# Kernel tuning notes

Measured on AMD Instinct MI355X. Metric: run time of the kernel, lower is better.

## Reference

```python
import jax, jax.numpy as jnp
import numpy as np

SHIFT = 8  # shift_range init kwarg
EPS = 1e-12  # F.normalize default eps (x / max(||x||, eps))


def setup_inputs() -> dict:
    key = jax.random.key(0)
    k1, k2 = jax.random.split(key)
    grd_feature = jax.random.normal(k1, (64, 64, 24, 24), dtype=jnp.float32)
    sat_feature = jax.random.normal(k2, (64, 64, 64, 64), dtype=jnp.float32)
    return {"grd_feature": grd_feature, "sat_feature": sat_feature}


def reference(grd_feature, sat_feature):
    M, C, Hs, Ws = sat_feature.shape
    N, _, H, W = grd_feature.shape
    kH = min(H, Hs - 2 * SHIFT, 24)
    kW = min(W, Ws - 2 * SHIFT, 24)
    # center-crop ground features to kernel size
    grd = grd_feature[:, :, H // 2 - kH // 2: H // 2 + kH // 2,
                      W // 2 - kW // 2: W // 2 + kW // 2]  # [N,C,kH,kW]
    # crop sat features to search window (kernel + 2*shift)
    sat = sat_feature[:, :, Hs // 2 - SHIFT - kH // 2: Hs // 2 + SHIFT + kH // 2,
                      Ws // 2 - SHIFT - kW // 2: Ws // 2 + SHIFT + kW // 2]  # [M,C,Hi,Wi]
    # cross-correlation: repeat+grouped-conv in torch == plain conv2d here -> [M,N,Ho,Wo]
    corr = jax.lax.conv_general_dilated(
        sat, grd, window_strides=(1, 1), padding='VALID',
        dimension_numbers=('NCHW', 'OIHW', 'NCHW'))
    Ho, Wo = corr.shape[2], corr.shape[3]
    flat_idx = jnp.argmax(corr.reshape(M, N, Ho * Wo), axis=-1)  # [M,N]
    hy = flat_idx // Wo
    wx = flat_idx % Wo

    def gather_patch(sat_j, h, w):  # sat_j: [C,Hi,Wi]
        return jax.lax.dynamic_slice(sat_j, (0, h, w), (C, kH, kW))

    # vectorized patch gather over (M, N) -> [M,N,C,kH,kW]
    patches = jax.vmap(
        lambda sj, hs, ws: jax.vmap(lambda h, w: gather_patch(sj, h, w))(hs, ws)
    )(sat, hy, wx)

    pn = patches.reshape(M * N, -1)
    pn = pn / jnp.maximum(jnp.linalg.norm(pn, axis=-1, keepdims=True), EPS)
    pn = pn.reshape(M, N, C, kH, kW)
    gn = grd.reshape(N, -1)
    gn = gn / jnp.maximum(jnp.linalg.norm(gn, axis=-1, keepdims=True), EPS)
    gn = gn.reshape(N, C, kH, kW)
    similarity_matrix = jnp.einsum('mnchw,nchw->mn', pn, gn)
    sat_f = patches[M - 1, N - 1]  # last gathered (unnormalized) patch, as in torch
    return similarity_matrix, sat_f
```

## Files before the change

kernel.cpp:

```cpp
#include <hip/hip_runtime.h>
#include <hip/hip_bf16.h>
#include <math.h>


typedef float f32x16 __attribute__((ext_vector_type(16)));
typedef short short8 __attribute__((ext_vector_type(8)));

#define SATT_H 0u
#define GRDT_H 3276800u
#define CORR_O 4456448u
#define WING_O 5701632u
#define GN2_O  5702016u
#define CEX_O  5702144u
#define S2G_O  5702528u

__global__ __launch_bounds__(256) void prep(const float* __restrict__ sat,
                                            const float* __restrict__ grd,
                                            __hip_bfloat16* __restrict__ sth,
                                            __hip_bfloat16* __restrict__ gth,
                                            float* __restrict__ S2g,
                                            float* __restrict__ gn2p,
                                            float* __restrict__ corrz) {
    __shared__ __hip_bfloat16 shb[32 * 577];
    int bid = blockIdx.x;
    int tid = threadIdx.x;

    if (bid < 2560) {
        {
            int f4 = bid * 122 + tid;
            if (tid < 122 && f4 < 311392)
                ((float4*)corrz)[f4] = make_float4(0.f, 0.f, 0.f, 0.f);
        }
        int m = bid / 40, r = bid % 40;
        const float* base = sat + (size_t)m * 262144 + (12 + r) * 64 + 12;
        for (int k = 0; k < 10; k++) {
            int idx = tid + 256 * k;
            int c = idx / 40, w2 = idx % 40;
            shb[w2 * 66 + c] = __float2bfloat16(base[c * 4096 + w2]);
        }
        __syncthreads();
        __hip_bfloat16* dh = sth + (size_t)m * 102400 + r * 640;
        for (int k = 0; k < 10; k++) {
            int idx = tid + 256 * k;
            int cc = idx / 640, rem = idx - cc * 640;
            int w2 = rem >> 4, cl = rem & 15;
            dh[cc * 25600 + w2 * 16 + cl] = shb[w2 * 66 + cc * 16 + cl];
        }
        if (tid < 40) {
            float s = 0.0f;
            for (int c = 0; c < 64; c++) {
                float v = __bfloat162float(shb[tid * 66 + c]);
                s += v * v;
            }
            S2g[m * 1600 + r * 40 + tid] = s;
        }
    } else {
        __shared__ float red[4];
        int x = bid - 2560;
        int n = x >> 1, ch = x & 1;
        const float* src = grd + (size_t)n * 36864 + ch * 32 * 576;
        float s = 0.0f;
        for (int k = 0; k < 72; k++) {
            int idx = tid + 256 * k;
            int cl = idx / 576, ij = idx % 576;
            float v = src[idx];
            s += v * v;
            shb[cl * 577 + ij] = __float2bfloat16(v);
        }
        for (int off = 32; off; off >>= 1) s += __shfl_down(s, off);
        if ((tid & 63) == 0) red[tid >> 6] = s;
        __syncthreads();
        if (tid == 0) gn2p[ch * 64 + n] = red[0] + red[1] + red[2] + red[3];
        for (int k = 0; k < 72; k++) {
            int idx = tid + 256 * k;
            int ij = idx >> 5, cl = idx & 31;
            int c = ch * 32 + cl;
            gth[((size_t)((c >> 4) * 576 + ij)) * 1024 + n * 16 + (c & 15)] = shb[cl * 577 + ij];
        }
    }
}

__global__ __launch_bounds__(256, 2) void corr_mfma(const __hip_bfloat16* __restrict__ sth,
                                                    const __hip_bfloat16* __restrict__ gth,
                                                    float* __restrict__ corr,
                                                    const float* __restrict__ sat,
                                                    const float* __restrict__ grd,
                                                    float* __restrict__ correx) {
    __shared__ __align__(16) __hip_bfloat16 satW[760 * 16];

    int bid = blockIdx.x;
    int tid = threadIdx.x;

    if (bid >= 512) {
        int p = bid - 512;
        int hy = p / 17, wx = p % 17;
        const float* satm = sat + (size_t)63 * 262144;
        const float* grdn = grd + (size_t)63 * 36864;
        float dot = 0.0f;
        for (int e = tid; e < 36864; e += 256) {
            int c = e / 576, rem = e - c * 576;
            int i = rem / 24, j = rem - i * 24;
            dot += satm[c * 4096 + (12 + hy + i) * 64 + 12 + wx + j] * grdn[e];
        }
        for (int off = 32; off; off >>= 1) dot += __shfl_down(dot, off);
        float* red = (float*)satW;
        if ((tid & 63) == 0) red[tid >> 6] = dot;
        __syncthreads();
        if (tid == 0) correx[p] = red[0] + red[1] + red[2] + red[3];
        return;
    }

    int xcd = bid & 7, slot = bid >> 3;
    int m = xcd * 8 + (slot >> 3), iq = slot & 7;
    int w = tid >> 6, l = tid & 63;
    int ln31 = l & 31, h = l >> 5;

    int rowbase[3];
#pragma unroll
    for (int t = 0; t < 3; t++) {
        int p = (w + 4 * t) * 32 + ln31;
        if (p > 288) p = 288;
        rowbase[t] = (p / 17) * 40 + (p % 17);
    }
    f32x16 acc[3][2];
#pragma unroll
    for (int t = 0; t < 3; t++) {
        acc[t][0] = (f32x16)0.0f;
        acc[t][1] = (f32x16)0.0f;
    }

    const __hip_bfloat16* gbase = gth + (size_t)(iq * 72) * 1024 + ln31 * 16 + h * 8;

#define BLOADR(B0, B1, CC, IJL) {                                               \
        const __hip_bfloat16* p_ = gbase + ((size_t)(CC) * 576 + (IJL)) * 1024; \
        B0 = *(const short8*)p_;                                                \
        B1 = *(const short8*)(p_ + 512);                                        \
    }
#define COMPUTE(IJL, B0, B1) {                                                  \
        int il_ = (IJL) / 24;                                                   \
        int pixoff_ = il_ * 40 + ((IJL) - il_ * 24);                            \
        __builtin_amdgcn_s_setprio(1);                                          \
        if (w < 2) {                                                            \
            _Pragma("unroll")                                                   \
            for (int t = 0; t < 3; t++) {                                       \
                int ao = (rowbase[t] + pixoff_) * 32 + h * 16;                  \
                short8 af = *(const short8*)((const char*)satW + ao);           \
                acc[t][0] = __builtin_amdgcn_mfma_f32_32x32x16_bf16(af, B0, acc[t][0], 0, 0, 0); \
                acc[t][1] = __builtin_amdgcn_mfma_f32_32x32x16_bf16(af, B1, acc[t][1], 0, 0, 0); \
            }                                                                   \
        } else {                                                                \
            _Pragma("unroll")                                                   \
            for (int t = 0; t < 2; t++) {                                       \
                int ao = (rowbase[t] + pixoff_) * 32 + h * 16;                  \
                short8 af = *(const short8*)((const char*)satW + ao);           \
                acc[t][0] = __builtin_amdgcn_mfma_f32_32x32x16_bf16(af, B0, acc[t][0], 0, 0, 0); \
                acc[t][1] = __builtin_amdgcn_mfma_f32_32x32x16_bf16(af, B1, acc[t][1], 0, 0, 0); \
            }                                                                   \
        }                                                                       \
        __builtin_amdgcn_s_setprio(0);                                          \
    }

#pragma unroll
    for (int cc = 0; cc < 4; cc++) {
        __syncthreads();
        const __hip_bfloat16* satb = sth + (size_t)m * 102400 + cc * 25600 + iq * 1920;
#pragma unroll
        for (int k2 = 0; k2 < 6; k2++) {
            int s = tid + 256 * k2;
            if (s < 1520) {
                float4 v = *(const float4*)(satb + s * 8);
                *(float4*)((char*)satW + s * 16) = v;
            }
        }
        short8 x0, x1, y0, y1, z0, z1;
        BLOADR(x0, x1, cc, 0);
        BLOADR(y0, y1, cc, 1);
        BLOADR(z0, z1, cc, 2);
        __syncthreads();

        for (int ijg = 0; ijg < 24; ijg++) {
            int base = ijg * 3;
            COMPUTE(base + 0, x0, x1);
            if (base + 3 < 72) BLOADR(x0, x1, cc, base + 3);
            COMPUTE(base + 1, y0, y1);
            if (base + 4 < 72) BLOADR(y0, y1, cc, base + 4);
            COMPUTE(base + 2, z0, z1);
            if (base + 5 < 72) BLOADR(z0, z1, cc, base + 5);
        }
    }

    int T = (w < 2) ? 3 : 2;
#pragma unroll
    for (int t = 0; t < 3; t++) {
        if (t >= T) break;
        int tile = w + 4 * t;
#pragma unroll
        for (int nt = 0; nt < 2; nt++)
#pragma unroll
            for (int q = 0; q < 16; q++) {
                int prow = tile * 32 + (q & 3) + 8 * (q >> 2) + 4 * h;
                if (prow < 289)
                    atomicAdd(&corr[((size_t)m * 304 + prow) * 64 + nt * 32 + ln31],
                              acc[t][nt][q]);
            }
    }
#undef BLOADR
#undef COMPUTE
}

__global__ __launch_bounds__(256) void argsim(const float* __restrict__ corr,
                                              const float* __restrict__ S2g,
                                              const float* __restrict__ gn2p,
                                              float* __restrict__ winG,
                                              float* __restrict__ out) {
    __shared__ float S2[40][41];
    __shared__ float RS[40][18];
    __shared__ float w2[304];
    __shared__ float gn[64];
    __shared__ float fbv[4][64];
    __shared__ int   fbi[4][64];
    int m = blockIdx.x, tid = threadIdx.x;
    for (int k = 0; k < 7; k++) {
        int idx = tid + 256 * k;
        if (idx < 1600) S2[idx / 40][idx % 40] = S2g[m * 1600 + idx];
    }
    if (tid < 64) gn[tid] = gn2p[tid] + gn2p[64 + tid];
    __syncthreads();
    for (int k = 0; k < 3; k++) {
        int idx = tid + 256 * k;
        if (idx < 680) {
            int r = idx / 17, x = idx % 17;
            float s = 0.0f;
            for (int j = 0; j < 24; j++) s += S2[r][x + j];
            RS[r][x] = s;
        }
    }
    __syncthreads();
    for (int k = 0; k < 2; k++) {
        int idx = tid + 256 * k;
        if (idx < 289) {
            int y = idx / 17, x = idx % 17;
            float s = 0.0f;
            for (int i2 = 0; i2 < 24; i2++) s += RS[y + i2][x];
            w2[idx] = s;
            if (m == 63) winG[idx] = s;
        }
    }
    __syncthreads();
    int n = tid & 63, pg = tid >> 6;
    float bv = -3.0e38f;
    int bi = 1 << 30;
    for (int p = pg; p < 289; p += 4) {
        float v = corr[((size_t)m * 304 + p) * 64 + n];
        if (v > bv) { bv = v; bi = p; }
    }
    fbv[pg][n] = bv;
    fbi[pg][n] = bi;
    __syncthreads();
    if (pg == 0) {
        for (int q = 1; q < 4; q++) {
            float ov = fbv[q][n];
            int oi = fbi[q][n];
            if (ov > bv || (ov == bv && oi < bi)) { bv = ov; bi = oi; }
        }
        out[m * 64 + n] = bv / (fmaxf(sqrtf(w2[bi]), 1e-12f) * fmaxf(sqrtf(gn[n]), 1e-12f));
    }
}

__global__ __launch_bounds__(256) void copy_patch(const float* __restrict__ sat,
                                                  const float* __restrict__ cex,
                                                  const float* __restrict__ winG,
                                                  const float* __restrict__ gn2p,
                                                  float* __restrict__ out) {
    __shared__ float rbv[4];
    __shared__ int rbi[4];
    int tid = threadIdx.x;
    float bv = -3.0e38f;
    int bi = 1 << 30;
    for (int p = tid; p < 289; p += 256) {
        float v = cex[p];
        if (v > bv) { bv = v; bi = p; }
    }
    for (int off = 32; off; off >>= 1) {
        float ov = __shfl_down(bv, off);
        int oi = __shfl_down(bi, off);
        if (ov > bv || (ov == bv && oi < bi)) { bv = ov; bi = oi; }
    }
    if ((tid & 63) == 0) { rbv[tid >> 6] = bv; rbi[tid >> 6] = bi; }
    __syncthreads();
    if (tid == 0) {
        for (int q = 1; q < 4; q++)
            if (rbv[q] > rbv[0] || (rbv[q] == rbv[0] && rbi[q] < rbi[0])) {
                rbv[0] = rbv[q]; rbi[0] = rbi[q];
            }
        if (blockIdx.x == 0) {
            float gn63 = gn2p[63] + gn2p[127];
            out[4095] = rbv[0] / (fmaxf(sqrtf(winG[rbi[0]]), 1e-12f) *
                                  fmaxf(sqrtf(gn63), 1e-12f));
        }
    }
    __syncthreads();
    int fidx = rbi[0];
    int hy = fidx / 17, wx = fidx % 17;
    int e = blockIdx.x * 256 + tid;
    int c = e / 576;
    int rem = e - c * 576;
    int rr = rem / 24, col = rem - rr * 24;
    out[4096 + e] = sat[(size_t)(63 * 64 + c) * 4096 + (12 + hy + rr) * 64 + 12 + wx + col];
}

extern "C" void kernel_launch(void* const* d_in, const int* in_sizes, int n_in,
                              void* d_out, int out_size, void* d_ws, size_t ws_size,
                              hipStream_t stream) {
    const float* grd = (const float*)d_in[0];
    const float* sat = (const float*)d_in[1];
    float* out = (float*)d_out;

    float* wsf = (float*)d_ws;
    __hip_bfloat16* sth = (__hip_bfloat16*)(wsf + SATT_H);
    __hip_bfloat16* gth = (__hip_bfloat16*)(wsf + GRDT_H);
    float* corr = wsf + CORR_O;
    float* winG = wsf + WING_O;
    float* gn2p = wsf + GN2_O;
    float* cex  = wsf + CEX_O;
    float* S2g  = wsf + S2G_O;

    prep<<<2688, 256, 0, stream>>>(sat, grd, sth, gth, S2g, gn2p, corr);
    corr_mfma<<<801, 256, 0, stream>>>(sth, gth, corr, sat, grd, cex);
    argsim<<<64, 256, 0, stream>>>(corr, S2g, gn2p, winG, out);
    copy_patch<<<144, 256, 0, stream>>>(sat, cex, winG, gn2p, out);
}
```

Before: 180.8 us.

## Split exact fp32 correlation for m=63 into its own kernel and drop setprio

Moves the 289 extra blocks that compute exact fp32 correlations for the last satellite out of corr_mfma into a separate exact63 kernel launched before it. Each thread now computes whole 24-wide rows with unrolled FMAs over contiguous memory instead of element-wise index math with divisions. The s_setprio bracketing around the MFMA sections is also removed. The intent is to make the exact path cheaper and keep the MFMA kernel uniform, at the cost of an extra serialized launch on the stream.

```diff
diff --git a/kernel.cpp b/kernel.cpp
--- a/kernel.cpp
+++ b/kernel.cpp
@@ -82,36 +82,13 @@
 
 __global__ __launch_bounds__(256, 2) void corr_mfma(const __hip_bfloat16* __restrict__ sth,
                                                     const __hip_bfloat16* __restrict__ gth,
-                                                    float* __restrict__ corr,
-                                                    const float* __restrict__ sat,
-                                                    const float* __restrict__ grd,
-                                                    float* __restrict__ correx) {
+                                                    float* __restrict__ corr) {
     __shared__ __align__(16) __hip_bfloat16 satW[760 * 16];
 
     int bid = blockIdx.x;
-    int tid = threadIdx.x;
-
-    if (bid >= 512) {
-        int p = bid - 512;
-        int hy = p / 17, wx = p % 17;
-        const float* satm = sat + (size_t)63 * 262144;
-        const float* grdn = grd + (size_t)63 * 36864;
-        float dot = 0.0f;
-        for (int e = tid; e < 36864; e += 256) {
-            int c = e / 576, rem = e - c * 576;
-            int i = rem / 24, j = rem - i * 24;
-            dot += satm[c * 4096 + (12 + hy + i) * 64 + 12 + wx + j] * grdn[e];
-        }
-        for (int off = 32; off; off >>= 1) dot += __shfl_down(dot, off);
-        float* red = (float*)satW;
-        if ((tid & 63) == 0) red[tid >> 6] = dot;
-        __syncthreads();
-        if (tid == 0) correx[p] = red[0] + red[1] + red[2] + red[3];
-        return;
-    }
-
     int xcd = bid & 7, slot = bid >> 3;
     int m = xcd * 8 + (slot >> 3), iq = slot & 7;
+    int tid = threadIdx.x;
     int w = tid >> 6, l = tid & 63;
     int ln31 = l & 31, h = l >> 5;
 
@@ -139,7 +116,6 @@
 #define COMPUTE(IJL, B0, B1) {                                                  \
         int il_ = (IJL) / 24;                                                   \
         int pixoff_ = il_ * 40 + ((IJL) - il_ * 24);                            \
-        __builtin_amdgcn_s_setprio(1);                                          \
         if (w < 2) {                                                            \
             _Pragma("unroll")                                                   \
             for (int t = 0; t < 3; t++) {                                       \
@@ -157,7 +133,6 @@
                 acc[t][1] = __builtin_amdgcn_mfma_f32_32x32x16_bf16(af, B1, acc[t][1], 0, 0, 0); \
             }                                                                   \
         }                                                                       \
-        __builtin_amdgcn_s_setprio(0);                                          \
     }
 
 #pragma unroll
@@ -206,6 +181,35 @@
     }
 #undef BLOADR
 #undef COMPUTE
+}
+
+__global__ __launch_bounds__(256) void exact63(const float* __restrict__ sat,
+                                               const float* __restrict__ grd,
+                                               float* __restrict__ correx) {
+    int p = blockIdx.x;
+    int hy = p / 17, wx = p % 17;
+    int tid = threadIdx.x;
+    const float* satm = sat + (size_t)63 * 262144 + (12 + hy) * 64 + 12 + wx;
+    const float* grdn = grd + (size_t)63 * 36864;
+
+    float a[6];
+#pragma unroll
+    for (int k = 0; k < 6; k++) {
+        int row = tid + 256 * k;
+        int c = row / 24, i = row - c * 24;
+        const float* sp = satm + c * 4096 + i * 64;
+        const float* gp = grdn + row * 24;
+        float s = 0.0f;
+#pragma unroll
+        for (int j = 0; j < 24; j++) s = fmaf(sp[j], gp[j], s);
+        a[k] = s;
+    }
+    float dot = ((a[0] + a[1]) + (a[2] + a[3])) + (a[4] + a[5]);
+    for (int off = 32; off; off >>= 1) dot += __shfl_down(dot, off);
+    __shared__ float red[4];
+    if ((tid & 63) == 0) red[tid >> 6] = dot;
+    __syncthreads();
+    if (tid == 0) correx[p] = red[0] + red[1] + red[2] + red[3];
 }
 
 __global__ __launch_bounds__(256) void argsim(const float* __restrict__ corr,
@@ -326,7 +330,8 @@
     float* S2g  = wsf + S2G_O;
 
     prep<<<2688, 256, 0, stream>>>(sat, grd, sth, gth, S2g, gn2p, corr);
-    corr_mfma<<<801, 256, 0, stream>>>(sth, gth, corr, sat, grd, cex);
+    exact63<<<289, 256, 0, stream>>>(sat, grd, cex);
+    corr_mfma<<<512, 256, 0, stream>>>(sth, gth, corr);
     argsim<<<64, 256, 0, stream>>>(corr, S2g, gn2p, winG, out);
     copy_patch<<<144, 256, 0, stream>>>(sat, cex, winG, gn2p, out);
 }
```

Result: faster. 169.0 us, median of 2 (-6.5%).
